# Performance work log

Hardware: AMD Instinct MI355X
Metric: run time of the kernel (lower is better)

The kernel has to match this reference:

```python
import jax, jax.numpy as jnp
import numpy as np

D = 10000          # hypervector dimensionality (DIMENSIONS in source)
ALPHA = 0.85
MAX_ITER = 100
TOL = 1e-6


def _pagerank(edge_index, num_nodes):
    # sparse column-stochastic adjacency power iteration (faithful to source)
    row, col = edge_index[0], edge_index[1]
    ones = jnp.ones(edge_index.shape[1], dtype=jnp.float32)
    deg = jax.ops.segment_sum(ones, col, num_segments=num_nodes)  # bincount(columns)
    vals = ALPHA / deg[col]                                       # alpha / out-degree per edge
    p = jnp.float32(1.0 / num_nodes)

    def cond(state):
        v, err, i = state
        return jnp.logical_and(i < MAX_ITER, err >= num_nodes * TOL)

    def body(state):
        v, _, i = state
        mv = jax.ops.segment_sum(vals * v[col], row, num_segments=num_nodes)
        v_new = mv + p * (1.0 - ALPHA)
        return (v_new, jnp.abs(v_new - v).sum(), i + 1)

    v0 = jnp.full((num_nodes,), p, dtype=jnp.float32)
    v, _, _ = jax.lax.while_loop(cond, body, (v0, jnp.float32(jnp.inf), jnp.int32(0)))
    return v


def _undirected_unique(edge_index, num_nodes):
    # to_undirected: sort each edge's endpoints then unique columns.
    # jit-safe emulation: sort by scalar key, mask duplicate keys (weight 0).
    ei = jnp.sort(edge_index, axis=0)                 # [2, E], min/max per edge
    keys = ei[0] * num_nodes + ei[1]
    order = jnp.argsort(keys)
    ksort = keys[order]
    first = jnp.concatenate([jnp.ones((1,), bool), ksort[1:] != ksort[:-1]])
    mask = first.astype(jnp.float32)                  # 1.0 for unique edges, 0.0 for dups
    return ei[0][order], ei[1][order], mask


def setup_inputs() -> dict:
    key = jax.random.key(0)
    k1, k2, k3 = jax.random.split(key, 3)
    N, E, C = 2000, 8192, 10
    edge_index = jax.random.randint(k1, (2, E), 0, N, dtype=jnp.int64)
    # torchhd Random embedding: random bipolar {-1, +1} hypervectors
    node_ids_weight = jnp.where(jax.random.uniform(k2, (N, D)) < 0.5, -1.0, 1.0).astype(jnp.float32)
    # source inits classify weight to 0; use small random values so the output is non-degenerate
    classify_weight = jax.random.normal(k3, (C, D), dtype=jnp.float32) * 0.01
    return {"edge_index": edge_index, "node_ids_weight": node_ids_weight,
            "classify_weight": classify_weight, "num_nodes": N}


def reference(edge_index, node_ids_weight, classify_weight, num_nodes):
    pr = _pagerank(edge_index, num_nodes)
    pr_argsort = jnp.argsort(pr)
    # node_id_hvs[pr_argsort] = node_ids.weight[:num_nodes]
    node_id_hvs = jnp.zeros((num_nodes, D), dtype=node_ids_weight.dtype)
    node_id_hvs = node_id_hvs.at[pr_argsort].set(node_ids_weight[:num_nodes])
    row, col, mask = _undirected_unique(edge_index, num_nodes)
    # bind = elementwise multiply (MAP VSA); multiset = sum over (unique) edges
    enc = jnp.einsum('e,ed,ed->d', mask, node_id_hvs[row], node_id_hvs[col])
    return enc @ classify_weight.T   # Linear(D, num_classes, bias=False)
```

## Files before the change

kernel.cpp:

```cpp
#include <hip/hip_runtime.h>
#include <hip/hip_bf16.h>

#define NN 2000
#define NE 8192
#define DIM 10000
#define NCLS 10
#define WORDS 313
#define ECH 4
#define REGD 12
#define DUMMY 2047

#define WS_FLAG    0
#define WS_ENCP    64
#define WS_V       320576
#define WS_RANK    328576
#define WS_OWN     336576
#define WS_PACK    344768

#define SENT 0xD00DFEEDCAFEBABEULL
#define HSZ 16384

#define PACK_BLK 612
#define DED0  (1 + PACK_BLK)
#define RANK0 (DED0 + 1)
#define RANK_BLK 8
#define GRID1 (RANK0 + RANK_BLK)

__device__ __forceinline__ float wave_sum_dpp(float x) {
#define DPPADD(ctrl, rm, bm)                                                     \
  {                                                                              \
    int y_ = __builtin_amdgcn_update_dpp(0, __float_as_int(x), ctrl, rm, bm, false); \
    x = __fadd_rn(x, __int_as_float(y_));                                        \
  }
  DPPADD(0x111, 0xF, 0xF);
  DPPADD(0x112, 0xF, 0xF);
  DPPADD(0x114, 0xF, 0xE);
  DPPADD(0x118, 0xF, 0xC);
  DPPADD(0x142, 0xA, 0xF);
  DPPADD(0x143, 0xC, 0xF);
#undef DPPADD
  return x;
}

struct Blk0Smem {
  float4 s_red4[2][4];
  float s_wv[2][2048];
  unsigned short s_ccol[NE];
  unsigned short s_ced[NE];
  int s_base[NN + 1];
  int s_aux[2048];
  int s_w[2048];
};
struct RankSmem { float s_v[NN]; int s_part[4][256]; };

__global__ __launch_bounds__(1024) void fused_pre_kernel(const int* __restrict__ eidx,
                                                         const float* __restrict__ W,
                                                         char* __restrict__ ws) {
  __shared__ alignas(16) char smem[73680];
  int tid = threadIdx.x;
  int bid = blockIdx.x;

  if (bid >= 1 && bid <= PACK_BLK) {
    int t = (bid - 1) * 1024 + tid;
    if (t >= NN * WORDS) return;
    unsigned int* packed = (unsigned int*)(ws + WS_PACK);
    int w = t / NN;
    int node = t - w * NN;
    int d0 = w * 32;
    const float* p = W + (size_t)node * DIM + d0;
    unsigned int m = 0;
    if (d0 + 32 <= DIM) {
#pragma unroll
      for (int q = 0; q < 8; ++q) {
        float4 v4 = *reinterpret_cast<const float4*>(p + q * 4);
        m |= (__float_as_uint(v4.x) >> 31) << (q * 4);
        m |= (__float_as_uint(v4.y) >> 31) << (q * 4 + 1);
        m |= (__float_as_uint(v4.z) >> 31) << (q * 4 + 2);
        m |= (__float_as_uint(v4.w) >> 31) << (q * 4 + 3);
      }
    } else {
      for (int q = 0; q < DIM - d0; ++q) m |= (__float_as_uint(p[q]) >> 31) << q;
    }
    packed[(size_t)w * NN + node] = m;
    return;
  }

  if (bid == DED0) {
    int* s_hash = reinterpret_cast<int*>(smem);
    unsigned char* own8 = (unsigned char*)(ws + WS_OWN);
    for (int i = tid; i < HSZ; i += 1024) s_hash[i] = -1;
    __syncthreads();
#pragma unroll
    for (int k = 0; k < 8; ++k) {
      int e = tid + k * 1024;
      int r = eidx[e], c = eidx[NE + e];
      int a = min(r, c), b = max(r, c);
      int key = a * NN + b;
      unsigned int h = ((unsigned int)key * 2654435761u) >> 18;
      unsigned char o;
      for (;;) {
        h &= (HSZ - 1);
        int old = atomicCAS(&s_hash[h], -1, key);
        if (old == -1) { o = 1; break; }
        if (old == key) { o = 0; break; }
        ++h;
      }
      own8[e] = o;
    }
    return;
  }

  if (bid >= RANK0) {
    RankSmem* S = reinterpret_cast<RankSmem*>(smem);
    unsigned long long* flag = (unsigned long long*)(ws + WS_FLAG);
    if (tid == 0) {
      while (__hip_atomic_load(flag, __ATOMIC_ACQUIRE, __HIP_MEMORY_SCOPE_AGENT) != SENT)
        __builtin_amdgcn_s_sleep(8);
    }
    __syncthreads();
    const float* v = (const float*)(ws + WS_V);
    int* rnk = (int*)(ws + WS_RANK);
    for (int j = tid; j < NN; j += 1024) S->s_v[j] = v[j];
    __syncthreads();
    int li = tid & 255;
    int seg = tid >> 8;
    int i = (bid - RANK0) * 256 + li;
    float vi = (i < NN) ? S->s_v[i] : 0.f;
    const int jper = NN / 4;
    int j0 = seg * jper, j1 = j0 + jper;
    int r = 0;
    for (int j = j0; j < j1; ++j) {
      float vj = S->s_v[j];
      r += ((vj < vi) || (vj == vi && j < i)) ? 1 : 0;
    }
    S->s_part[seg][li] = r;
    __syncthreads();
    if (tid < 256) {
      int i2 = (bid - RANK0) * 256 + tid;
      if (i2 < NN)
        rnk[i2] = S->s_part[0][tid] + S->s_part[1][tid] + S->s_part[2][tid] + S->s_part[3][tid];
    }
    return;
  }

  Blk0Smem* S = reinterpret_cast<Blk0Smem*>(smem);
  unsigned short* s_ccol = S->s_ccol;
  unsigned short* s_ced = S->s_ced;
  int* s_base = S->s_base;
  int* s_aux = S->s_aux;
  int* s_w = S->s_w;
  float* s_redf = (float*)S->s_red4;
  float* s_val = (float*)s_aux;

  int wid = tid >> 6, lane = tid & 63;

  for (int i = tid; i < 2048; i += 1024) { s_w[i] = 0; s_aux[i] = 0; }
  for (int i = NN + tid; i < 2048; i += 1024) { S->s_wv[0][i] = 0.f; S->s_wv[1][i] = 0.f; }
  __syncthreads();

  int er[8], ec[8];
#pragma unroll
  for (int k = 0; k < 8; ++k) {
    int e = tid + k * 1024;
    er[k] = eidx[e];
    ec[k] = eidx[NE + e];
    atomicAdd(&s_w[er[k]], 1);
    atomicAdd(&s_aux[ec[k]], 1);
  }
  __syncthreads();

  {
    int n0 = tid, n1 = tid + 1024;
    for (int st = 1; st < 2048; st <<= 1) {
      int v0 = (n0 >= st) ? s_w[n0 - st] : 0;
      int v1 = (n1 >= st) ? s_w[n1 - st] : 0;
      __syncthreads();
      s_w[n0] += v0;
      s_w[n1] += v1;
      __syncthreads();
    }
    if (tid == 0) s_base[0] = 0;
    for (int n = tid; n < NN; n += 1024) s_base[n + 1] = s_w[n];
  }
  __syncthreads();
  for (int i = tid; i < 2048; i += 1024) s_w[i] = 0;
  __syncthreads();

#pragma unroll
  for (int k = 0; k < 8; ++k) {
    int e = tid + k * 1024;
    int r = er[k];
    int slot = s_base[r] + atomicAdd(&s_w[r], 1);
    s_ccol[slot] = (unsigned short)ec[k];
    s_ced[slot] = (unsigned short)e;
  }
  __syncthreads();

  const float p = 0.0005f;
  const float addv = 0.0005f * 0.15f;
  for (int n = tid; n < NN; n += 1024) {
    int s0 = s_base[n], s1 = s_base[n + 1];
    for (int a = s0 + 1; a < s1; ++a) {
      unsigned short ke = s_ced[a], kc = s_ccol[a];
      int b = a - 1;
      while (b >= s0 && s_ced[b] > ke) {
        s_ced[b + 1] = s_ced[b];
        s_ccol[b + 1] = s_ccol[b];
        --b;
      }
      s_ced[b + 1] = ke;
      s_ccol[b + 1] = kc;
    }
    float vv = 0.85f / (float)s_aux[n];
    s_val[n] = vv;
    S->s_wv[0][n] = __fmul_rn(vv, p);
  }
  __syncthreads();

  bool own = (tid < 512);
  int r0 = tid, r1 = tid + 512, r2 = tid + 1024, r3 = tid + 1536;
  bool has3 = own && (r3 < NN);
  int b0s = 0, b0e = 0, b1s = 0, b1e = 0, b2s = 0, b2e = 0, b3s = 0, b3e = 0;
  float val0 = 0.f, val1 = 0.f, val2 = 0.f, val3 = 0.f;
  if (own) {
    b0s = s_base[r0]; b0e = s_base[r0 + 1];
    b1s = s_base[r1]; b1e = s_base[r1 + 1];
    b2s = s_base[r2]; b2e = s_base[r2 + 1];
    val0 = s_val[r0]; val1 = s_val[r1]; val2 = s_val[r2];
    if (has3) { b3s = s_base[r3]; b3e = s_base[r3 + 1]; val3 = s_val[r3]; }
  }
  int c0r[REGD], c1r[REGD], c2r[REGD], c3r[REGD];
#pragma unroll
  for (int k = 0; k < REGD; ++k) {
    c0r[k] = (own && b0s + k < b0e) ? (int)s_ccol[min(b0s + k, NE - 1)] : DUMMY;
    c1r[k] = (own && b1s + k < b1e) ? (int)s_ccol[min(b1s + k, NE - 1)] : DUMMY;
    c2r[k] = (own && b2s + k < b2e) ? (int)s_ccol[min(b2s + k, NE - 1)] : DUMMY;
    c3r[k] = (has3 && b3s + k < b3e) ? (int)s_ccol[min(b3s + k, NE - 1)] : DUMMY;
  }
  float vc0 = p, vc1 = p, vc2 = p, vc3 = p;

#define ROW_SUM(CR, BS, BE, VN)                                                \
  {                                                                            \
    float sum = 0.f;                                                           \
    _Pragma("unroll")                                                          \
    for (int k = 0; k < REGD; ++k) sum = __fadd_rn(sum, wv[CR[k]]);            \
    for (int k = (BS) + REGD; k < (BE); ++k) sum = __fadd_rn(sum, wv[s_ccol[k]]); \
    VN = __fadd_rn(sum, addv);                                                 \
  }

  float err = __builtin_inff();
  int it = 0;
  int pb = 0;
  while (it < 100 && err >= 0.002f) {
    const float* wv = S->s_wv[pb];
    float ep = 0.f;
    float vn0 = vc0, vn1 = vc1, vn2 = vc2, vn3 = vc3;
    if (own) {
      ROW_SUM(c0r, b0s, b0e, vn0); ep += fabsf(__fsub_rn(vn0, vc0));
      ROW_SUM(c1r, b1s, b1e, vn1); ep += fabsf(__fsub_rn(vn1, vc1));
      ROW_SUM(c2r, b2s, b2e, vn2); ep += fabsf(__fsub_rn(vn2, vc2));
      if (has3) { ROW_SUM(c3r, b3s, b3e, vn3); ep += fabsf(__fsub_rn(vn3, vc3)); }
      float* wvn = S->s_wv[pb ^ 1];
      wvn[r0] = __fmul_rn(val0, vn0);
      wvn[r1] = __fmul_rn(val1, vn1);
      wvn[r2] = __fmul_rn(val2, vn2);
      if (has3) wvn[r3] = __fmul_rn(val3, vn3);
    }
    vc0 = vn0; vc1 = vn1; vc2 = vn2; vc3 = vn3;
    float wsum = wave_sum_dpp(ep);
    if (lane == 63) s_redf[pb * 16 + wid] = wsum;
    __syncthreads();
    float4 q0 = S->s_red4[pb][0], q1 = S->s_red4[pb][1];
    float4 q2 = S->s_red4[pb][2], q3 = S->s_red4[pb][3];
    float t = 0.f;
    t += q0.x; t += q0.y; t += q0.z; t += q0.w;
    t += q1.x; t += q1.y; t += q1.z; t += q1.w;
    t += q2.x; t += q2.y; t += q2.z; t += q2.w;
    t += q3.x; t += q3.y; t += q3.z; t += q3.w;
    err = t;
    pb ^= 1;
    ++it;
  }
#undef ROW_SUM
  float* vout = (float*)(ws + WS_V);
  if (own) {
    vout[r0] = vc0;
    vout[r1] = vc1;
    vout[r2] = vc2;
    if (has3) vout[r3] = vc3;
  }
  __syncthreads();
  if (tid == 0) {
    unsigned long long* flag = (unsigned long long*)(ws + WS_FLAG);
    __hip_atomic_store(flag, SENT, __ATOMIC_RELEASE, __HIP_MEMORY_SCOPE_AGENT);
  }
}

__global__ __launch_bounds__(256) void encpop_kernel(const int* __restrict__ eidx,
                                                     char* __restrict__ ws) {
  const unsigned int* packed = (const unsigned int*)(ws + WS_PACK);
  const int* rnk_g = (const int*)(ws + WS_RANK);
  const unsigned char* own8 = (const unsigned char*)(ws + WS_OWN);
  int* encp = (int*)(ws + WS_ENCP);
  __shared__ unsigned int s_col[NN];
  __shared__ int s_part[4][32];
  int w = blockIdx.x;
  int tid = threadIdx.x;
  int wid = tid >> 6, lane = tid & 63;
  for (int i = tid; i < NN; i += 256)
    s_col[i] = packed[(size_t)w * NN + rnk_g[i]];
  __syncthreads();
  const int per = NE / ECH;
  int e0 = blockIdx.y * per;
  int cnt[32];
#pragma unroll
  for (int b = 0; b < 32; ++b) cnt[b] = 0;
  for (int e = e0 + tid; e < e0 + per; e += 256) {
    unsigned int x = 0;
    if (own8[e]) {
      int r = eidx[e], c = eidx[NE + e];
      int a = min(r, c), b2 = max(r, c);
      x = s_col[a] ^ s_col[b2];
    }
#pragma unroll
    for (int b = 0; b < 32; ++b)
      cnt[b] += (int)__popcll(__ballot(x & (1u << b)));
  }
  if (lane == 0) {
#pragma unroll
    for (int b = 0; b < 32; ++b) s_part[wid][b] = cnt[b];
  }
  __syncthreads();
  if (tid < 32) {
    int tot = s_part[0][tid] + s_part[1][tid] + s_part[2][tid] + s_part[3][tid];
    encp[blockIdx.y * 10016 + w * 32 + tid] = tot;
  }
}

__global__ __launch_bounds__(256) void out_kernel(const float* __restrict__ Wc,
                                                  char* __restrict__ ws,
                                                  float* __restrict__ out) {
  const int* encp = (const int*)(ws + WS_ENCP);
  const unsigned char* own8 = (const unsigned char*)(ws + WS_OWN);
  __shared__ float red[4];
  __shared__ int redi[4];
  __shared__ int s_K;
  int tid = threadIdx.x;
  int c = blockIdx.x;
  int kk = 0;
  for (int i = tid; i < NE; i += 256) kk += own8[i];
  for (int o = 32; o > 0; o >>= 1) kk += __shfl_down(kk, o, 64);
  if ((tid & 63) == 0) redi[tid >> 6] = kk;
  __syncthreads();
  if (tid == 0) s_K = redi[0] + redi[1] + redi[2] + redi[3];
  __syncthreads();
  int K = s_K;
  float s = 0.f;
  for (int d = tid; d < DIM; d += 256) {
    int cnt = encp[d] + encp[10016 + d] + encp[2 * 10016 + d] + encp[3 * 10016 + d];
    s += (float)(K - 2 * cnt) * Wc[c * DIM + d];
  }
  for (int o = 32; o > 0; o >>= 1) s += __shfl_down(s, o, 64);
  if ((tid & 63) == 0) red[tid >> 6] = s;
  __syncthreads();
  if (tid == 0) out[c] = red[0] + red[1] + red[2] + red[3];
}

extern "C" void kernel_launch(void* const* d_in, const int* in_sizes, int n_in,
                              void* d_out, int out_size, void* d_ws, size_t ws_size,
                              hipStream_t stream) {
  const int* eidx = (const int*)d_in[0];
  const float* Wn = (const float*)d_in[1];
  const float* Wc = (const float*)d_in[2];
  float* out = (float*)d_out;
  char* ws = (char*)d_ws;

  fused_pre_kernel<<<GRID1, 1024, 0, stream>>>(eidx, Wn, ws);
  encpop_kernel<<<dim3(WORDS, ECH), 256, 0, stream>>>(eidx, ws);
  out_kernel<<<NCLS, 256, 0, stream>>>(Wc, ws, out);
}
```

Measured before the change: 72.89 us.

## Fuse popcount encoding with classifier projection and drop edge chunking

Merges the per-word popcount kernel with the final linear projection. Each block now processes all edges for its 32 dimensions, computes the bipolar encoding directly, and atomically adds its partial dot products into the output. The output is zeroed in the pre-kernel. This removes one kernel launch and the intermediate count buffer round-trip, but each block does four times more edge work with only 313 blocks, and it adds float atomics with nondeterministic summation order.

```diff
diff --git a/kernel.cpp b/kernel.cpp
--- a/kernel.cpp
+++ b/kernel.cpp
@@ -6,12 +6,10 @@
 #define DIM 10000
 #define NCLS 10
 #define WORDS 313
-#define ECH 4
 #define REGD 12
 #define DUMMY 2047
 
 #define WS_FLAG    0
-#define WS_ENCP    64
 #define WS_V       320576
 #define WS_RANK    328576
 #define WS_OWN     336576
@@ -55,7 +53,8 @@
 
 __global__ __launch_bounds__(1024) void fused_pre_kernel(const int* __restrict__ eidx,
                                                          const float* __restrict__ W,
-                                                         char* __restrict__ ws) {
+                                                         char* __restrict__ ws,
+                                                         float* __restrict__ out) {
   __shared__ alignas(16) char smem[73680];
   int tid = threadIdx.x;
   int bid = blockIdx.x;
@@ -88,6 +87,7 @@
   if (bid == DED0) {
     int* s_hash = reinterpret_cast<int*>(smem);
     unsigned char* own8 = (unsigned char*)(ws + WS_OWN);
+    if (tid < NCLS) out[tid] = 0.f;
     for (int i = tid; i < HSZ; i += 1024) s_hash[i] = -1;
     __syncthreads();
 #pragma unroll
@@ -296,28 +296,32 @@
   }
 }
 
-__global__ __launch_bounds__(256) void encpop_kernel(const int* __restrict__ eidx,
-                                                     char* __restrict__ ws) {
+__global__ __launch_bounds__(256) void encpop_out_kernel(const int* __restrict__ eidx,
+                                                         const float* __restrict__ Wc,
+                                                         char* __restrict__ ws,
+                                                         float* __restrict__ out) {
   const unsigned int* packed = (const unsigned int*)(ws + WS_PACK);
   const int* rnk_g = (const int*)(ws + WS_RANK);
   const unsigned char* own8 = (const unsigned char*)(ws + WS_OWN);
-  int* encp = (int*)(ws + WS_ENCP);
   __shared__ unsigned int s_col[NN];
   __shared__ int s_part[4][32];
+  __shared__ int s_ki[4];
+  __shared__ float s_enc[32];
   int w = blockIdx.x;
   int tid = threadIdx.x;
   int wid = tid >> 6, lane = tid & 63;
   for (int i = tid; i < NN; i += 256)
     s_col[i] = packed[(size_t)w * NN + rnk_g[i]];
   __syncthreads();
-  const int per = NE / ECH;
-  int e0 = blockIdx.y * per;
   int cnt[32];
 #pragma unroll
   for (int b = 0; b < 32; ++b) cnt[b] = 0;
-  for (int e = e0 + tid; e < e0 + per; e += 256) {
+  int kk = 0;
+  for (int e = tid; e < NE; e += 256) {
     unsigned int x = 0;
-    if (own8[e]) {
+    int o = own8[e];
+    kk += o;
+    if (o) {
       int r = eidx[e], c = eidx[NE + e];
       int a = min(r, c), b2 = max(r, c);
       x = s_col[a] ^ s_col[b2];
@@ -326,44 +330,30 @@
     for (int b = 0; b < 32; ++b)
       cnt[b] += (int)__popcll(__ballot(x & (1u << b)));
   }
+  for (int o = 32; o > 0; o >>= 1) kk += __shfl_down(kk, o, 64);
   if (lane == 0) {
+    s_ki[wid] = kk;
 #pragma unroll
     for (int b = 0; b < 32; ++b) s_part[wid][b] = cnt[b];
   }
   __syncthreads();
   if (tid < 32) {
+    int K = s_ki[0] + s_ki[1] + s_ki[2] + s_ki[3];
     int tot = s_part[0][tid] + s_part[1][tid] + s_part[2][tid] + s_part[3][tid];
-    encp[blockIdx.y * 10016 + w * 32 + tid] = tot;
-  }
-}
-
-__global__ __launch_bounds__(256) void out_kernel(const float* __restrict__ Wc,
-                                                  char* __restrict__ ws,
-                                                  float* __restrict__ out) {
-  const int* encp = (const int*)(ws + WS_ENCP);
-  const unsigned char* own8 = (const unsigned char*)(ws + WS_OWN);
-  __shared__ float red[4];
-  __shared__ int redi[4];
-  __shared__ int s_K;
-  int tid = threadIdx.x;
-  int c = blockIdx.x;
-  int kk = 0;
-  for (int i = tid; i < NE; i += 256) kk += own8[i];
-  for (int o = 32; o > 0; o >>= 1) kk += __shfl_down(kk, o, 64);
-  if ((tid & 63) == 0) redi[tid >> 6] = kk;
-  __syncthreads();
-  if (tid == 0) s_K = redi[0] + redi[1] + redi[2] + redi[3];
-  __syncthreads();
-  int K = s_K;
-  float s = 0.f;
-  for (int d = tid; d < DIM; d += 256) {
-    int cnt = encp[d] + encp[10016 + d] + encp[2 * 10016 + d] + encp[3 * 10016 + d];
-    s += (float)(K - 2 * cnt) * Wc[c * DIM + d];
-  }
-  for (int o = 32; o > 0; o >>= 1) s += __shfl_down(s, o, 64);
-  if ((tid & 63) == 0) red[tid >> 6] = s;
-  __syncthreads();
-  if (tid == 0) out[c] = red[0] + red[1] + red[2] + red[3];
+    s_enc[tid] = (float)(K - 2 * tot);
+  }
+  __syncthreads();
+  if (tid < 64) {
+    int b = tid & 31;
+    int d = w * 32 + b;
+    float encb = (tid < 32 && d < DIM) ? s_enc[b] : 0.f;
+#pragma unroll
+    for (int c = 0; c < NCLS; ++c) {
+      float v = (tid < 32 && d < DIM) ? encb * Wc[c * DIM + d] : 0.f;
+      for (int o = 32; o > 0; o >>= 1) v += __shfl_down(v, o, 64);
+      if (tid == 0) atomicAdd(&out[c], v);
+    }
+  }
 }
 
 extern "C" void kernel_launch(void* const* d_in, const int* in_sizes, int n_in,
@@ -375,7 +365,6 @@
   float* out = (float*)d_out;
   char* ws = (char*)d_ws;
 
-  fused_pre_kernel<<<GRID1, 1024, 0, stream>>>(eidx, Wn, ws);
-  encpop_kernel<<<dim3(WORDS, ECH), 256, 0, stream>>>(eidx, ws);
-  out_kernel<<<NCLS, 256, 0, stream>>>(Wc, ws, out);
+  fused_pre_kernel<<<GRID1, 1024, 0, stream>>>(eidx, Wn, ws, out);
+  encpop_out_kernel<<<WORDS, 256, 0, stream>>>(eidx, Wc, ws, out);
 }
```

New measurement: 112.2 us. +53.9%, slower.
